# Performance work log

Hardware: AMD Instinct MI355X
Metric: run time of the kernel (lower is better)

Reference implementation:

```python
import jax, jax.numpy as jnp
import numpy as np

B, T, C, H = 2, 2048, 1024, 16
D = C // H
EPS = 1e-5
ROPE_BASE = 10000.0


def _rope_tables(t, d, base=ROPE_BASE):
    half = d // 2
    inv_freq = 1.0 / (base ** (jnp.arange(half, dtype=jnp.float32) / half))
    freqs = jnp.arange(t, dtype=jnp.float32)[:, None] * inv_freq[None, :]  # [T, D/2]
    emb = jnp.concatenate([freqs, freqs], axis=-1)  # [T, D]
    return jnp.cos(emb), jnp.sin(emb)


def _rotate_half(x):
    a, b = jnp.split(x, 2, axis=-1)
    return jnp.concatenate([-b, a], axis=-1)


def setup_inputs() -> dict:
    key = jax.random.key(0)
    k0, k1, k2 = jax.random.split(key, 3)
    s = 0.02  # typical init scale
    return {
        "x": jax.random.normal(k0, (B, T, C), jnp.float32),
        "attention_mask": jnp.ones((B, T), jnp.int32),
        "w_qkv": jax.random.normal(k1, (3 * C, C), jnp.float32) * s,
        "b_qkv": jnp.zeros((3 * C,), jnp.float32),
        "w_o": jax.random.normal(k2, (C, C), jnp.float32) * s,
        "b_o": jnp.zeros((C,), jnp.float32),
        "rms_w": jnp.ones((C,), jnp.float32),
    }


def reference(x, attention_mask, w_qkv, b_qkv, w_o, b_o, rms_w):
    b, t, c = x.shape
    h = H
    d = c // h
    # RMSNorm
    xn = x * jax.lax.rsqrt(jnp.mean(x * x, axis=-1, keepdims=True) + EPS) * rms_w
    # fused QKV projection -> [B, T, 3, H, D]
    qkv = (jnp.einsum('btc,oc->bto', xn, w_qkv) + b_qkv).reshape(b, t, 3, h, d)
    q, k, v = qkv[:, :, 0], qkv[:, :, 1], qkv[:, :, 2]
    # RoPE (position_ids = arange(T))
    cos, sin = _rope_tables(t, d)
    cos = cos[None, :, None, :]  # [1, T, 1, D]
    sin = sin[None, :, None, :]
    q = q * cos + _rotate_half(q) * sin
    k = k * cos + _rotate_half(k) * sin
    # causal attention (flash_attn_func semantics: scale 1/sqrt(d), causal)
    scores = jnp.einsum('bqhd,bkhd->bhqk', q, k) / jnp.sqrt(jnp.float32(d))
    causal = jnp.tril(jnp.ones((t, t), dtype=bool))
    scores = jnp.where(causal[None, None], scores, jnp.float32(-1e30))
    attn = jax.nn.softmax(scores, axis=-1)
    out = jnp.einsum('bhqk,bkhd->bqhd', attn, v).reshape(b, t, c)
    return jnp.einsum('btc,oc->bto', out, w_o) + b_o
```

## Files before the change

kernel.cpp:

```cpp
#include <hip/hip_runtime.h>
#include <math.h>

constexpr int Bb = 2;
constexpr int Tt = 2048;
constexpr int Cc = 1024;
constexpr int Hh = 16;
constexpr int M_ROWS = Bb * Tt;
constexpr float EPSV = 1e-5f;

typedef __attribute__((ext_vector_type(4))) float f32x4;
typedef __attribute__((ext_vector_type(8))) __bf16 bf16x8;
using u16 = unsigned short;

union Frag8 {
    u16 u[8];
    unsigned int ui[4];
    uint4 v;
    bf16x8 b;
};

__device__ __forceinline__ u16 f2bf(float f) {
    union { float f; unsigned int u; } c;
    c.f = f;
    unsigned int r = (c.u + 0x7fffu + ((c.u >> 16) & 1u)) >> 16;
    return (u16)r;
}
__device__ __forceinline__ float bf2f(u16 u) {
    union { unsigned int i; float f; } c;
    c.i = ((unsigned int)u) << 16;
    return c.f;
}

__device__ __forceinline__ void gload_lds16(const void* g, void* l) {
    __builtin_amdgcn_global_load_lds(
        (__attribute__((address_space(1))) void*)const_cast<void*>(g),
        (__attribute__((address_space(3))) void*)l, 16, 0, 0);
}

__global__ __launch_bounds__(256) void prep_k(const float* __restrict__ w_qkv,
                                              u16* __restrict__ wqkv_bf,
                                              const float* __restrict__ w_o,
                                              u16* __restrict__ wo_bf,
                                              float* __restrict__ cosT,
                                              float* __restrict__ sinT,
                                              const float* __restrict__ x,
                                              const float* __restrict__ rms_w,
                                              u16* __restrict__ xn) {
    __shared__ float ws_[4];
    int blk = blockIdx.x;
    int tid = threadIdx.x;
    if (blk < 3072) {
        int i = (blk * 256 + tid) * 4;
        float4 v = *(const float4*)&w_qkv[i];
        ushort4 o;
        o.x = f2bf(v.x); o.y = f2bf(v.y); o.z = f2bf(v.z); o.w = f2bf(v.w);
        *(ushort4*)&wqkv_bf[i] = o;
    } else if (blk < 4096) {
        int i = ((blk - 3072) * 256 + tid) * 4;
        float4 v = *(const float4*)&w_o[i];
        ushort4 o;
        o.x = f2bf(v.x); o.y = f2bf(v.y); o.z = f2bf(v.z); o.w = f2bf(v.w);
        *(ushort4*)&wo_bf[i] = o;
    } else if (blk < 4352) {
        int lin = (blk - 4096) * 256 + tid;
        int tt = lin >> 5, j = lin & 31;
        float inv = exp2f(-(float)j * (log2f(10000.0f) / 32.0f));
        float a = (float)tt * inv;
        cosT[lin] = cosf(a);
        sinT[lin] = sinf(a);
    } else {
        int row = blk - 4352;
        const float* xr = x + (size_t)row * Cc;
        float4 v = *(const float4*)&xr[tid * 4];
        float ss = v.x * v.x + v.y * v.y + v.z * v.z + v.w * v.w;
        #pragma unroll
        for (int off = 32; off > 0; off >>= 1) ss += __shfl_down(ss, off);
        if ((tid & 63) == 0) ws_[tid >> 6] = ss;
        __syncthreads();
        float tot = ws_[0] + ws_[1] + ws_[2] + ws_[3];
        float r = rsqrtf(tot * (1.0f / (float)Cc) + EPSV);
        float4 wv = *(const float4*)&rms_w[tid * 4];
        ushort4 o;
        o.x = f2bf(v.x * r * wv.x);
        o.y = f2bf(v.y * r * wv.y);
        o.z = f2bf(v.z * r * wv.z);
        o.w = f2bf(v.w * r * wv.w);
        *(ushort4*)&xn[(size_t)row * Cc + tid * 4] = o;
    }
}

template<bool BF16OUT>
__global__ __launch_bounds__(256) void gemm_mfma_k(const u16* __restrict__ A,
                                                   const u16* __restrict__ W,
                                                   const float* __restrict__ bias,
                                                   void* __restrict__ Ov,
                                                   int M, int N, int K) {
    __shared__ __align__(16) u16 As[128 * 64];
    __shared__ __align__(16) u16 Bs[64 * 64];

    const int tid = threadIdx.x;
    const int w = tid >> 6;
    const int l = tid & 63;
    const int wr = w >> 1;
    const int wc = w & 1;
    const int q = l & 15;
    const int g = l >> 4;

    const int m0 = blockIdx.y * 128;
    const int n0 = blockIdx.x * 64;

    const int srow = l >> 3;
    const int cph = l & 7;
    const int cl = cph ^ srow;

    f32x4 acc[4][2];
    #pragma unroll
    for (int i = 0; i < 4; ++i)
        #pragma unroll
        for (int j = 0; j < 2; ++j)
            acc[i][j] = (f32x4){0.f, 0.f, 0.f, 0.f};

    const int nkt = K >> 6;
    for (int kt = 0; kt < nkt; ++kt) {
        const int k0 = kt << 6;
        __syncthreads();
        #pragma unroll
        for (int iss = 0; iss < 4; ++iss) {
            int r = w * 32 + iss * 8 + srow;
            gload_lds16(A + (size_t)(m0 + r) * K + k0 + cl * 8,
                        &As[(w * 32 + iss * 8) * 64]);
        }
        #pragma unroll
        for (int iss = 0; iss < 2; ++iss) {
            int r = w * 16 + iss * 8 + srow;
            gload_lds16(W + (size_t)(n0 + r) * K + k0 + cl * 8,
                        &Bs[(w * 16 + iss * 8) * 64]);
        }
        __syncthreads();

        #pragma unroll
        for (int kk = 0; kk < 2; ++kk) {
            Frag8 af[4], bf[2];
            const int ca = kk * 4 + g;
            #pragma unroll
            for (int i = 0; i < 4; ++i) {
                int ra = wr * 64 + i * 16 + q;
                af[i] = *(const Frag8*)&As[ra * 64 + ((ca ^ (ra & 7)) * 8)];
            }
            #pragma unroll
            for (int j = 0; j < 2; ++j) {
                int rb = wc * 32 + j * 16 + q;
                bf[j] = *(const Frag8*)&Bs[rb * 64 + ((ca ^ (rb & 7)) * 8)];
            }
            #pragma unroll
            for (int i = 0; i < 4; ++i)
                #pragma unroll
                for (int j = 0; j < 2; ++j)
                    acc[i][j] = __builtin_amdgcn_mfma_f32_16x16x32_bf16(
                        af[i].b, bf[j].b, acc[i][j], 0, 0, 0);
        }
    }

    #pragma unroll
    for (int i = 0; i < 4; ++i) {
        int row = m0 + wr * 64 + i * 16 + g * 4;
        #pragma unroll
        for (int j = 0; j < 2; ++j) {
            int col = n0 + wc * 32 + j * 16 + q;
            float bb = bias[col];
            #pragma unroll
            for (int r2 = 0; r2 < 4; ++r2) {
                float val = acc[i][j][r2] + bb;
                if (BF16OUT)
                    ((u16*)Ov)[(size_t)(row + r2) * N + col] = f2bf(val);
                else
                    ((float*)Ov)[(size_t)(row + r2) * N + col] = val;
            }
        }
    }
}

__global__ __launch_bounds__(256) void rope_pack_k(const u16* __restrict__ qkv,
                                                   const float* __restrict__ cosT,
                                                   const float* __restrict__ sinT,
                                                   u16* __restrict__ Qb,
                                                   u16* __restrict__ Kb,
                                                   u16* __restrict__ Vt) {
    const int t0 = blockIdx.x * 64;
    const int h = blockIdx.y, b = blockIdx.z;
    const int t = threadIdx.x;
    const int bh = b * Hh + h;
    __shared__ u16 Vs[64 * 64];
    constexpr float QSC = 0.125f * 1.44269504089f;

    {
        int row = t >> 2, d16 = (t & 3) * 16;
        const u16* vp = qkv + (size_t)(b * Tt + t0 + row) * 3072 + 2048 + h * 64 + d16;
        *(uint4*)&Vs[row * 64 + d16]     = *(const uint4*)vp;
        *(uint4*)&Vs[row * 64 + d16 + 8] = *(const uint4*)(vp + 8);
    }

    {
        int row = t >> 2, d0 = (t & 3) * 8;
        size_t rb = (size_t)(b * Tt + t0 + row) * 3072 + h * 64;
        const u16* qp = qkv + rb;
        const u16* kp = qkv + rb + 1024;
        Frag8 qlo, qhi, klo, khi;
        qlo.v = *(const uint4*)&qp[d0];
        qhi.v = *(const uint4*)&qp[d0 + 32];
        klo.v = *(const uint4*)&kp[d0];
        khi.v = *(const uint4*)&kp[d0 + 32];
        const float* cp = &cosT[(t0 + row) * 32 + d0];
        const float* sp = &sinT[(t0 + row) * 32 + d0];
        float4 c0 = *(const float4*)cp, c1 = *(const float4*)(cp + 4);
        float4 s0 = *(const float4*)sp, s1 = *(const float4*)(sp + 4);
        float cc[8] = {c0.x, c0.y, c0.z, c0.w, c1.x, c1.y, c1.z, c1.w};
        float ss[8] = {s0.x, s0.y, s0.z, s0.w, s1.x, s1.y, s1.z, s1.w};
        Frag8 oql, oqh, okl, okh;
        #pragma unroll
        for (int i = 0; i < 8; ++i) {
            float ql = bf2f(qlo.u[i]), qh = bf2f(qhi.u[i]);
            float kl = bf2f(klo.u[i]), kh = bf2f(khi.u[i]);
            oql.u[i] = f2bf((ql * cc[i] - qh * ss[i]) * QSC);
            oqh.u[i] = f2bf((qh * cc[i] + ql * ss[i]) * QSC);
            okl.u[i] = f2bf(kl * cc[i] - kh * ss[i]);
            okh.u[i] = f2bf(kh * cc[i] + kl * ss[i]);
        }
        u16* qd = Qb + ((size_t)bh * Tt + t0 + row) * 64;
        u16* kd = Kb + ((size_t)bh * Tt + t0 + row) * 64;
        *(uint4*)&qd[d0]      = oql.v;
        *(uint4*)&qd[d0 + 32] = oqh.v;
        *(uint4*)&kd[d0]      = okl.v;
        *(uint4*)&kd[d0 + 32] = okh.v;
    }
    __syncthreads();

    {
        int d = t >> 2, kq = (t & 3) * 16;
        Frag8 a, b2;
        #pragma unroll
        for (int j = 0; j < 16; ++j) {
            int slot = kq + j;
            int key = ((slot >> 5) * 2 + ((slot >> 2) & 1)) * 16
                    + ((slot >> 3) & 3) * 4 + (slot & 3);
            u16 vv = Vs[key * 64 + d];
            if (j < 8) a.u[j] = vv; else b2.u[j - 8] = vv;
        }
        u16* vd = Vt + ((size_t)bh * 64 + d) * Tt + t0 + kq;
        *(uint4*)&vd[0] = a.v;
        *(uint4*)&vd[8] = b2.v;
    }
}

__global__ __launch_bounds__(512) void attn_mfma_k(const u16* __restrict__ Qb,
                                                   const u16* __restrict__ Kb,
                                                   const u16* __restrict__ Vt,
                                                   u16* __restrict__ out) {
    const int i = blockIdx.x;
    int c, bh;
    if (i < 512) { c = 31 - (i >> 5); bh = i & 31; }
    else         { int k = i - 512; c = k >> 5; bh = k & 31; }
    const int b = bh >> 4, h = bh & 15;

    const int t = threadIdx.x;
    const int w = t >> 6;
    const int team = w >> 2;
    const int w4 = w & 3;
    const int l = t & 63;
    const int q15 = l & 15;
    const int g2 = l >> 4;

    __shared__ __align__(16) char lds[32768];
    u16* Ksm = (u16*)(lds + team * 8192);
    u16* Vsm = (u16*)(lds + 16384 + team * 8192);
    float* red = (float*)lds;

    const int nj = c + 1;
    const int h0 = (nj + 1) >> 1;
    const int myn = team ? (nj - h0) : h0;
    const int jbase = team ? h0 : 0;

    Frag8 qf[2];
    {
        int qrow = c * 64 + w4 * 16 + q15;
        const u16* qp = Qb + ((size_t)bh * Tt + qrow) * 64;
        qf[0] = *(const Frag8*)&qp[g2 * 8];
        qf[1] = *(const Frag8*)&qp[32 + g2 * 8];
    }

    Frag8 ones;
    #pragma unroll
    for (int e = 0; e < 8; ++e) ones.u[e] = 0x3F80;

    f32x4 acco[4];
    #pragma unroll
    for (int dg = 0; dg < 4; ++dg) acco[dg] = (f32x4){0.f, 0.f, 0.f, 0.f};
    f32x4 acc_l = (f32x4){0.f, 0.f, 0.f, 0.f};

    const int srow = l >> 3;
    const int cph = l & 7;
    const int xsw = cph ^ srow;
    const u16* Kbase = Kb + (size_t)bh * Tt * 64;
    const u16* Vbase = Vt + (size_t)bh * 64 * Tt;

    for (int it = 0; it < h0; ++it) {
        __syncthreads();
        const int j = jbase + it;
        if (it < myn) {
            #pragma unroll
            for (int iss = 0; iss < 2; ++iss) {
                int rr = w4 * 16 + iss * 8 + srow;
                gload_lds16(Kbase + (size_t)(j * 64 + rr) * 64 + xsw * 8,
                            &Ksm[(w4 * 16 + iss * 8) * 64]);
                gload_lds16(Vbase + (size_t)rr * Tt + j * 64 + xsw * 8,
                            &Vsm[(w4 * 16 + iss * 8) * 64]);
            }
        }
        __syncthreads();
        if (it < myn) {
            f32x4 sacc[4];
            __builtin_amdgcn_s_setprio(1);
            #pragma unroll
            for (int g = 0; g < 4; ++g) {
                sacc[g] = (f32x4){0.f, 0.f, 0.f, 0.f};
                int krow = g * 16 + q15;
                #pragma unroll
                for (int kk = 0; kk < 2; ++kk) {
                    Frag8 kf = *(const Frag8*)&Ksm[krow * 64 + (((kk * 4 + g2) ^ (krow & 7)) * 8)];
                    sacc[g] = __builtin_amdgcn_mfma_f32_16x16x32_bf16(
                        kf.b, qf[kk].b, sacc[g], 0, 0, 0);
                }
            }
            __builtin_amdgcn_s_setprio(0);
            if (j == c) {
                #pragma unroll
                for (int g = 0; g < 4; ++g)
                    #pragma unroll
                    for (int r = 0; r < 4; ++r)
                        if (g * 16 + g2 * 4 + r > w4 * 16 + q15) sacc[g][r] = -1e30f;
            }

            Frag8 pa[2];
            #pragma unroll
            for (int kk = 0; kk < 2; ++kk)
                #pragma unroll
                for (int e = 0; e < 8; ++e)
                    pa[kk].b[e] = (__bf16)exp2f(sacc[2 * kk + (e >> 2)][e & 3]);

            __builtin_amdgcn_s_setprio(1);
            acc_l = __builtin_amdgcn_mfma_f32_16x16x32_bf16(pa[0].b, ones.b, acc_l, 0, 0, 0);
            acc_l = __builtin_amdgcn_mfma_f32_16x16x32_bf16(pa[1].b, ones.b, acc_l, 0, 0, 0);
            #pragma unroll
            for (int dg = 0; dg < 4; ++dg) {
                int vrow = dg * 16 + q15;
                #pragma unroll
                for (int kk = 0; kk < 2; ++kk) {
                    Frag8 vf = *(const Frag8*)&Vsm[vrow * 64 + (((kk * 4 + g2) ^ (vrow & 7)) * 8)];
                    acco[dg] = __builtin_amdgcn_mfma_f32_16x16x32_bf16(
                        pa[kk].b, vf.b, acco[dg], 0, 0, 0);
                }
            }
            __builtin_amdgcn_s_setprio(0);
        }
    }

    __syncthreads();
    const int slot = (w4 * 64 + l) * 20;
    if (team == 1) {
        #pragma unroll
        for (int dg = 0; dg < 4; ++dg)
            #pragma unroll
            for (int r = 0; r < 4; ++r) red[slot + dg * 4 + r] = acco[dg][r];
        #pragma unroll
        for (int r = 0; r < 4; ++r) red[slot + 16 + r] = acc_l[r];
    }
    __syncthreads();
    if (team == 0) {
        #pragma unroll
        for (int dg = 0; dg < 4; ++dg)
            #pragma unroll
            for (int r = 0; r < 4; ++r) acco[dg][r] += red[slot + dg * 4 + r];
        #pragma unroll
        for (int r = 0; r < 4; ++r) acc_l[r] += red[slot + 16 + r];

        float lr[4];
        #pragma unroll
        for (int r = 0; r < 4; ++r) lr[r] = 1.f / acc_l[r];
        const int qbase = c * 64 + w4 * 16;
        #pragma unroll
        for (int dg = 0; dg < 4; ++dg)
            #pragma unroll
            for (int r = 0; r < 4; ++r)
                out[((size_t)(b * Tt + qbase + g2 * 4 + r)) * Cc + h * 64 + dg * 16 + q15] =
                    f2bf(acco[dg][r] * lr[r]);
    }
}

extern "C" void kernel_launch(void* const* d_in, const int* in_sizes, int n_in,
                              void* d_out, int out_size, void* d_ws, size_t ws_size,
                              hipStream_t stream) {
    const float* x      = (const float*)d_in[0];
    const float* w_qkv  = (const float*)d_in[2];
    const float* b_qkv  = (const float*)d_in[3];
    const float* w_o    = (const float*)d_in[4];
    const float* b_o    = (const float*)d_in[5];
    const float* rms_w  = (const float*)d_in[6];
    float* out = (float*)d_out;

    char* ws = (char*)d_ws;
    u16*   xn_bf   = (u16*)ws;
    u16*   Kb      = (u16*)(ws + (size_t)(8 << 20));
    u16*   Vt      = (u16*)(ws + (size_t)(16 << 20));
    u16*   Qb      = (u16*)(ws + (size_t)(24 << 20));
    u16*   qkvb    = (u16*)(ws + (size_t)(32 << 20));
    u16*   wqkv_bf = (u16*)(ws + (size_t)(56 << 20));
    u16*   wo_bf   = (u16*)(ws + (size_t)(62 << 20));
    float* cosT    = (float*)(ws + (size_t)(64 << 20));
    float* sinT    = (float*)(ws + (size_t)(64 << 20) + (1 << 18));
    u16*   attn_bf = xn_bf;

    prep_k<<<dim3(8448), dim3(256), 0, stream>>>(w_qkv, wqkv_bf, w_o, wo_bf,
                                                 cosT, sinT, x, rms_w, xn_bf);
    gemm_mfma_k<true><<<dim3(3 * Cc / 64, M_ROWS / 128), dim3(256), 0, stream>>>(
        xn_bf, wqkv_bf, b_qkv, qkvb, M_ROWS, 3 * Cc, Cc);
    rope_pack_k<<<dim3(Tt / 64, Hh, Bb), dim3(256), 0, stream>>>(
        qkvb, cosT, sinT, Qb, Kb, Vt);
    attn_mfma_k<<<dim3(1024), dim3(512), 0, stream>>>(Qb, Kb, Vt, attn_bf);
    gemm_mfma_k<false><<<dim3(Cc / 64, M_ROWS / 128), dim3(256), 0, stream>>>(
        attn_bf, wo_bf, b_o, out, M_ROWS, Cc, Cc);
}
```

Baseline: 113.7 us.

## Pre-swizzle K/V into MFMA fragment order and load directly from global

The rope/pack kernel now writes K and V into per-64-key tiles laid out exactly in MFMA fragment order, so each lane reads its operand with one contiguous 16-byte load. The attention kernel drops LDS staging, barriers, and the two-team key split with LDS reduction. It uses 256 threads per block, each wave streaming K/V fragments straight from global/L2. This removes sync and LDS traffic but loses cross-wave sharing of K/V loads (four waves each reload the same tile) and the intra-block split of long causal rows.

After: 114.6 us. Within noise of the previous version (+0.7%).

```diff
diff --git a/kernel.cpp b/kernel.cpp
--- a/kernel.cpp
+++ b/kernel.cpp
@@ -184,14 +184,16 @@
                                                    const float* __restrict__ cosT,
                                                    const float* __restrict__ sinT,
                                                    u16* __restrict__ Qb,
-                                                   u16* __restrict__ Kb,
-                                                   u16* __restrict__ Vt) {
-    const int t0 = blockIdx.x * 64;
+                                                   u16* __restrict__ KL,
+                                                   u16* __restrict__ VL) {
+    const int jt = blockIdx.x;
+    const int t0 = jt * 64;
     const int h = blockIdx.y, b = blockIdx.z;
     const int t = threadIdx.x;
     const int bh = b * Hh + h;
     __shared__ u16 Vs[64 * 64];
     constexpr float QSC = 0.125f * 1.44269504089f;
+    const size_t tilebase = ((size_t)bh * 32 + jt) * 4096;
 
     {
         int row = t >> 2, d16 = (t & 3) * 16;
@@ -202,6 +204,7 @@
 
     {
         int row = t >> 2, d0 = (t & 3) * 8;
+        int g = row >> 4, q15 = row & 15, g2 = t & 3;
         size_t rb = (size_t)(b * Tt + t0 + row) * 3072 + h * 64;
         const u16* qp = qkv + rb;
         const u16* kp = qkv + rb + 1024;
@@ -227,16 +230,18 @@
             okh.u[i] = f2bf(kh * cc[i] + kl * ss[i]);
         }
         u16* qd = Qb + ((size_t)bh * Tt + t0 + row) * 64;
-        u16* kd = Kb + ((size_t)bh * Tt + t0 + row) * 64;
         *(uint4*)&qd[d0]      = oql.v;
         *(uint4*)&qd[d0 + 32] = oqh.v;
-        *(uint4*)&kd[d0]      = okl.v;
-        *(uint4*)&kd[d0 + 32] = okh.v;
+        *(uint4*)&KL[tilebase + (size_t)(0 * 4 + g) * 512 + (g2 * 16 + q15) * 8] = okl.v;
+        *(uint4*)&KL[tilebase + (size_t)(1 * 4 + g) * 512 + (g2 * 16 + q15) * 8] = okh.v;
     }
     __syncthreads();
 
     {
         int d = t >> 2, kq = (t & 3) * 16;
+        int dg = d >> 4, q15v = d & 15;
+        int kkv = (t & 3) >> 1;
+        int g2a = ((t & 3) & 1) * 2;
         Frag8 a, b2;
         #pragma unroll
         for (int j = 0; j < 16; ++j) {
@@ -246,15 +251,15 @@
             u16 vv = Vs[key * 64 + d];
             if (j < 8) a.u[j] = vv; else b2.u[j - 8] = vv;
         }
-        u16* vd = Vt + ((size_t)bh * 64 + d) * Tt + t0 + kq;
-        *(uint4*)&vd[0] = a.v;
-        *(uint4*)&vd[8] = b2.v;
-    }
-}
-
-__global__ __launch_bounds__(512) void attn_mfma_k(const u16* __restrict__ Qb,
-                                                   const u16* __restrict__ Kb,
-                                                   const u16* __restrict__ Vt,
+        u16* base = VL + tilebase + (size_t)(kkv * 4 + dg) * 512;
+        *(uint4*)&base[(g2a * 16 + q15v) * 8]       = a.v;
+        *(uint4*)&base[((g2a + 1) * 16 + q15v) * 8] = b2.v;
+    }
+}
+
+__global__ __launch_bounds__(256) void attn_mfma_k(const u16* __restrict__ Qb,
+                                                   const u16* __restrict__ KL,
+                                                   const u16* __restrict__ VL,
                                                    u16* __restrict__ out) {
     const int i = blockIdx.x;
     int c, bh;
@@ -263,22 +268,10 @@
     const int b = bh >> 4, h = bh & 15;
 
     const int t = threadIdx.x;
-    const int w = t >> 6;
-    const int team = w >> 2;
-    const int w4 = w & 3;
+    const int w4 = t >> 6;
     const int l = t & 63;
     const int q15 = l & 15;
     const int g2 = l >> 4;
-
-    __shared__ __align__(16) char lds[32768];
-    u16* Ksm = (u16*)(lds + team * 8192);
-    u16* Vsm = (u16*)(lds + 16384 + team * 8192);
-    float* red = (float*)lds;
-
-    const int nj = c + 1;
-    const int h0 = (nj + 1) >> 1;
-    const int myn = team ? (nj - h0) : h0;
-    const int jbase = team ? h0 : 0;
 
     Frag8 qf[2];
     {
@@ -297,103 +290,76 @@
     for (int dg = 0; dg < 4; ++dg) acco[dg] = (f32x4){0.f, 0.f, 0.f, 0.f};
     f32x4 acc_l = (f32x4){0.f, 0.f, 0.f, 0.f};
 
-    const int srow = l >> 3;
-    const int cph = l & 7;
-    const int xsw = cph ^ srow;
-    const u16* Kbase = Kb + (size_t)bh * Tt * 64;
-    const u16* Vbase = Vt + (size_t)bh * 64 * Tt;
-
-    for (int it = 0; it < h0; ++it) {
-        __syncthreads();
-        const int j = jbase + it;
-        if (it < myn) {
-            #pragma unroll
-            for (int iss = 0; iss < 2; ++iss) {
-                int rr = w4 * 16 + iss * 8 + srow;
-                gload_lds16(Kbase + (size_t)(j * 64 + rr) * 64 + xsw * 8,
-                            &Ksm[(w4 * 16 + iss * 8) * 64]);
-                gload_lds16(Vbase + (size_t)rr * Tt + j * 64 + xsw * 8,
-                            &Vsm[(w4 * 16 + iss * 8) * 64]);
-            }
-        }
-        __syncthreads();
-        if (it < myn) {
-            f32x4 sacc[4];
-            __builtin_amdgcn_s_setprio(1);
-            #pragma unroll
-            for (int g = 0; g < 4; ++g) {
-                sacc[g] = (f32x4){0.f, 0.f, 0.f, 0.f};
-                int krow = g * 16 + q15;
+    const u16* kp0 = KL + ((size_t)bh * 32) * 4096 + l * 8;
+    const u16* kp1 = kp0 + 2048;
+    const u16* vp0 = VL + ((size_t)bh * 32) * 4096 + l * 8;
+    const u16* vp1 = vp0 + 2048;
+
+    for (int j = 0; j <= c; ++j) {
+        Frag8 kf[2][4];
+        #pragma unroll
+        for (int g = 0; g < 4; ++g) {
+            kf[0][g] = *(const Frag8*)&kp0[g * 512];
+            kf[1][g] = *(const Frag8*)&kp1[g * 512];
+        }
+        f32x4 sacc[4];
+        __builtin_amdgcn_s_setprio(1);
+        #pragma unroll
+        for (int g = 0; g < 4; ++g) {
+            sacc[g] = (f32x4){0.f, 0.f, 0.f, 0.f};
+            sacc[g] = __builtin_amdgcn_mfma_f32_16x16x32_bf16(
+                kf[0][g].b, qf[0].b, sacc[g], 0, 0, 0);
+            sacc[g] = __builtin_amdgcn_mfma_f32_16x16x32_bf16(
+                kf[1][g].b, qf[1].b, sacc[g], 0, 0, 0);
+        }
+        __builtin_amdgcn_s_setprio(0);
+        if (j == c) {
+            #pragma unroll
+            for (int g = 0; g < 4; ++g)
                 #pragma unroll
-                for (int kk = 0; kk < 2; ++kk) {
-                    Frag8 kf = *(const Frag8*)&Ksm[krow * 64 + (((kk * 4 + g2) ^ (krow & 7)) * 8)];
-                    sacc[g] = __builtin_amdgcn_mfma_f32_16x16x32_bf16(
-                        kf.b, qf[kk].b, sacc[g], 0, 0, 0);
-                }
-            }
-            __builtin_amdgcn_s_setprio(0);
-            if (j == c) {
-                #pragma unroll
-                for (int g = 0; g < 4; ++g)
-                    #pragma unroll
-                    for (int r = 0; r < 4; ++r)
-                        if (g * 16 + g2 * 4 + r > w4 * 16 + q15) sacc[g][r] = -1e30f;
-            }
-
-            Frag8 pa[2];
-            #pragma unroll
-            for (int kk = 0; kk < 2; ++kk)
-                #pragma unroll
-                for (int e = 0; e < 8; ++e)
-                    pa[kk].b[e] = (__bf16)exp2f(sacc[2 * kk + (e >> 2)][e & 3]);
-
-            __builtin_amdgcn_s_setprio(1);
-            acc_l = __builtin_amdgcn_mfma_f32_16x16x32_bf16(pa[0].b, ones.b, acc_l, 0, 0, 0);
-            acc_l = __builtin_amdgcn_mfma_f32_16x16x32_bf16(pa[1].b, ones.b, acc_l, 0, 0, 0);
-            #pragma unroll
-            for (int dg = 0; dg < 4; ++dg) {
-                int vrow = dg * 16 + q15;
-                #pragma unroll
-                for (int kk = 0; kk < 2; ++kk) {
-                    Frag8 vf = *(const Frag8*)&Vsm[vrow * 64 + (((kk * 4 + g2) ^ (vrow & 7)) * 8)];
-                    acco[dg] = __builtin_amdgcn_mfma_f32_16x16x32_bf16(
-                        pa[kk].b, vf.b, acco[dg], 0, 0, 0);
-                }
-            }
-            __builtin_amdgcn_s_setprio(0);
-        }
-    }
-
-    __syncthreads();
-    const int slot = (w4 * 64 + l) * 20;
-    if (team == 1) {
-        #pragma unroll
-        for (int dg = 0; dg < 4; ++dg)
-            #pragma unroll
-            for (int r = 0; r < 4; ++r) red[slot + dg * 4 + r] = acco[dg][r];
-        #pragma unroll
-        for (int r = 0; r < 4; ++r) red[slot + 16 + r] = acc_l[r];
-    }
-    __syncthreads();
-    if (team == 0) {
-        #pragma unroll
-        for (int dg = 0; dg < 4; ++dg)
-            #pragma unroll
-            for (int r = 0; r < 4; ++r) acco[dg][r] += red[slot + dg * 4 + r];
-        #pragma unroll
-        for (int r = 0; r < 4; ++r) acc_l[r] += red[slot + 16 + r];
-
-        float lr[4];
-        #pragma unroll
-        for (int r = 0; r < 4; ++r) lr[r] = 1.f / acc_l[r];
-        const int qbase = c * 64 + w4 * 16;
-        #pragma unroll
-        for (int dg = 0; dg < 4; ++dg)
-            #pragma unroll
-            for (int r = 0; r < 4; ++r)
-                out[((size_t)(b * Tt + qbase + g2 * 4 + r)) * Cc + h * 64 + dg * 16 + q15] =
-                    f2bf(acco[dg][r] * lr[r]);
-    }
+                for (int r = 0; r < 4; ++r)
+                    if (g * 16 + g2 * 4 + r > w4 * 16 + q15) sacc[g][r] = -1e30f;
+        }
+
+        Frag8 pa[2];
+        #pragma unroll
+        for (int kk = 0; kk < 2; ++kk)
+            #pragma unroll
+            for (int e = 0; e < 8; ++e)
+                pa[kk].b[e] = (__bf16)exp2f(sacc[2 * kk + (e >> 2)][e & 3]);
+
+        Frag8 vf[2][4];
+        #pragma unroll
+        for (int dg = 0; dg < 4; ++dg) {
+            vf[0][dg] = *(const Frag8*)&vp0[dg * 512];
+            vf[1][dg] = *(const Frag8*)&vp1[dg * 512];
+        }
+        __builtin_amdgcn_s_setprio(1);
+        acc_l = __builtin_amdgcn_mfma_f32_16x16x32_bf16(pa[0].b, ones.b, acc_l, 0, 0, 0);
+        acc_l = __builtin_amdgcn_mfma_f32_16x16x32_bf16(pa[1].b, ones.b, acc_l, 0, 0, 0);
+        #pragma unroll
+        for (int dg = 0; dg < 4; ++dg) {
+            acco[dg] = __builtin_amdgcn_mfma_f32_16x16x32_bf16(
+                pa[0].b, vf[0][dg].b, acco[dg], 0, 0, 0);
+            acco[dg] = __builtin_amdgcn_mfma_f32_16x16x32_bf16(
+                pa[1].b, vf[1][dg].b, acco[dg], 0, 0, 0);
+        }
+        __builtin_amdgcn_s_setprio(0);
+
+        kp0 += 4096; kp1 += 4096;
+        vp0 += 4096; vp1 += 4096;
+    }
+
+    float lr[4];
+    #pragma unroll
+    for (int r = 0; r < 4; ++r) lr[r] = 1.f / acc_l[r];
+    const int qbase = c * 64 + w4 * 16;
+    #pragma unroll
+    for (int dg = 0; dg < 4; ++dg)
+        #pragma unroll
+        for (int r = 0; r < 4; ++r)
+            out[((size_t)(b * Tt + qbase + g2 * 4 + r)) * Cc + h * 64 + dg * 16 + q15] =
+                f2bf(acco[dg][r] * lr[r]);
 }
 
 extern "C" void kernel_launch(void* const* d_in, const int* in_sizes, int n_in,
@@ -409,8 +375,8 @@
 
     char* ws = (char*)d_ws;
     u16*   xn_bf   = (u16*)ws;
-    u16*   Kb      = (u16*)(ws + (size_t)(8 << 20));
-    u16*   Vt      = (u16*)(ws + (size_t)(16 << 20));
+    u16*   KL      = (u16*)(ws + (size_t)(8 << 20));
+    u16*   VL      = (u16*)(ws + (size_t)(16 << 20));
     u16*   Qb      = (u16*)(ws + (size_t)(24 << 20));
     u16*   qkvb    = (u16*)(ws + (size_t)(32 << 20));
     u16*   wqkv_bf = (u16*)(ws + (size_t)(56 << 20));
@@ -424,8 +390,8 @@
     gemm_mfma_k<true><<<dim3(3 * Cc / 64, M_ROWS / 128), dim3(256), 0, stream>>>(
         xn_bf, wqkv_bf, b_qkv, qkvb, M_ROWS, 3 * Cc, Cc);
     rope_pack_k<<<dim3(Tt / 64, Hh, Bb), dim3(256), 0, stream>>>(
-        qkvb, cosT, sinT, Qb, Kb, Vt);
-    attn_mfma_k<<<dim3(1024), dim3(512), 0, stream>>>(Qb, Kb, Vt, attn_bf);
+        qkvb, cosT, sinT, Qb, KL, VL);
+    attn_mfma_k<<<dim3(1024), dim3(256), 0, stream>>>(Qb, KL, VL, attn_bf);
     gemm_mfma_k<false><<<dim3(Cc / 64, M_ROWS / 128), dim3(256), 0, stream>>>(
         attn_bf, wo_bf, b_o, out, M_ROWS, Cc, Cc);
 }
```
